# Optimization experiments

Measured on AMD Instinct MI355X. Metric: run time of the kernel, lower is better.

Reference implementation:

```python
import jax, jax.numpy as jnp
import numpy as np

H = 768; NH = 12; HD = 64; LW = 256
NEG = -1e9  # finite stand-in for -inf; exp underflows to 0 identically in fp32 softmax

def setup_inputs() -> dict:
    key = jax.random.key(0)
    ks = jax.random.split(key, 10)
    s = 0.02
    return {
        "x": jax.random.normal(ks[0], (2, 2048, H), dtype=jnp.float32),
        "w_attn": jax.random.normal(ks[1], (H, 3 * H), dtype=jnp.float32) * s,
        "b_attn": jnp.zeros((3 * H,), dtype=jnp.float32),
        "w_proj": jax.random.normal(ks[2], (H, H), dtype=jnp.float32) * s,
        "b_proj": jnp.zeros((H,), dtype=jnp.float32),
        "w_sel1": jax.random.normal(ks[3], (H, H // 4), dtype=jnp.float32) * s,
        "b_sel1": jnp.zeros((H // 4,), dtype=jnp.float32),
        "w_sel2": jax.random.normal(ks[4], (H // 4, 1), dtype=jnp.float32) * s,
        "b_sel2": jnp.zeros((1,), dtype=jnp.float32),
        "local_weight": jnp.float32(0.5),
        "global_weight": jnp.float32(0.5),
    }

def reference(x, w_attn, b_attn, w_proj, b_proj, w_sel1, b_sel1, w_sel2, b_sel2,
              local_weight, global_weight):
    B, T, C = x.shape
    scale = HD ** -0.5
    qkv = x @ w_attn + b_attn                       # [B,T,3C]
    q, k, v = jnp.split(qkv, 3, axis=-1)
    q = q.reshape(B, T, NH, HD).transpose(0, 2, 1, 3)  # [B,H,T,D]
    k = k.reshape(B, T, NH, HD).transpose(0, 2, 1, 3)
    v = v.reshape(B, T, NH, HD).transpose(0, 2, 1, 3)
    scores = jnp.einsum('bhqd,bhkd->bhqk', q, k) * scale  # [B,H,T,T]
    i = jnp.arange(T)[:, None]
    j = jnp.arange(T)[None, :]
    causal = j > i
    scores = jnp.where(causal[None, None], NEG, scores)
    # selectivity: per-key-position gate in [0.2, 1.0]
    sel = jax.nn.sigmoid(jax.nn.gelu(x @ w_sel1 + b_sel1, approximate=False) @ w_sel2 + b_sel2)  # [B,T,1]
    sel = sel[:, None, :, 0][:, :, None, :]            # [B,1,1,T]
    modulated = scores * (0.2 + 0.8 * sel)
    outside_local = j < jnp.clip(i - LW, 0, None)
    local = jnp.where(outside_local[None, None], NEG, scores)
    wl = jax.nn.sigmoid(local_weight)
    wg = jax.nn.sigmoid(global_weight)
    wsum = wl + wg
    wl, wg = wl / wsum, wg / wsum
    attn = wl * jax.nn.softmax(local, axis=-1) + wg * jax.nn.softmax(modulated, axis=-1)
    out = jnp.einsum('bhqk,bhkd->bhqd', attn, v)        # [B,H,T,D]
    out = out.transpose(0, 2, 1, 3).reshape(B, T, C)
    return out @ w_proj + b_proj
```

## Files before the change

### kernel.cpp

```cpp
#include <hip/hip_runtime.h>
#include <cmath>

#define TT    2048
#define CC    768
#define NHEAD 12
#define LWIN  256
#define BBATCH 2
#define MROWS 4096
#define QBA   128
#define KB    64
#define NSLOT 72
#define L2E   1.4426950408889634f

typedef unsigned int u32;
typedef u32 u32x2 __attribute__((ext_vector_type(2)));
typedef u32 u32x4 __attribute__((ext_vector_type(4)));
typedef short bf16x8 __attribute__((ext_vector_type(8)));
typedef float f32x16 __attribute__((ext_vector_type(16)));

union F4 { u32x4 u; bf16x8 h; };

__device__ __forceinline__ unsigned short b16(float a) {
  u32 u = __float_as_uint(a);
  return (unsigned short)((u + 0x7FFFu + ((u >> 16) & 1u)) >> 16);
}
__device__ __forceinline__ u32 pk2(float a, float b) {
  return (u32)b16(a) | ((u32)b16(b) << 16);
}

__global__ __launch_bounds__(256) void cvt_bf16_kernel(
    const float* __restrict__ in, unsigned short* __restrict__ out, int n8) {
  const int i = blockIdx.x * 256 + threadIdx.x;
  if (i >= n8) return;
  const float4 a = *(const float4*)&in[(size_t)i * 8];
  const float4 b = *(const float4*)&in[(size_t)i * 8 + 4];
  u32x4 w = {pk2(a.x, a.y), pk2(a.z, a.w), pk2(b.x, b.y), pk2(b.z, b.w)};
  *(u32x4*)&out[(size_t)i * 8] = w;
}

__global__ __launch_bounds__(256) void transpose_cvt_kernel(
    const float* __restrict__ W, unsigned short* __restrict__ Wt, int K, int N) {
  __shared__ float t[32][33];
  const int tid = threadIdx.x;
  const int n0 = blockIdx.x * 32, k0 = blockIdx.y * 32;
  const int r = tid >> 5, c = tid & 31;
#pragma unroll
  for (int rr = 0; rr < 4; ++rr)
    t[r + 8 * rr][c] = W[(size_t)(k0 + r + 8 * rr) * N + n0 + c];
  __syncthreads();
#pragma unroll
  for (int rr = 0; rr < 4; ++rr)
    Wt[(size_t)(n0 + r + 8 * rr) * K + k0 + c] = b16(t[c][r + 8 * rr]);
}

template <int NT, bool OUTBF, int ACT>
__global__ __launch_bounds__(256) void gemm_mfma_kernel(
    const unsigned short* __restrict__ A, const unsigned short* __restrict__ Bt,
    const float* __restrict__ bias, void* __restrict__ Cout,
    int M, int N, int K) {
  __shared__ alignas(16) unsigned short as_[128 * 64];
  __shared__ alignas(16) unsigned short bs_[NT * 32 * 64];
  const int tid = threadIdx.x;
  const int lane = tid & 63;
  const int wv = tid >> 6;
  const int hi = lane >> 5;
  const int l31 = lane & 31;
  const int m0 = blockIdx.y * 128, n0 = blockIdx.x * (NT * 32);

  u32x4 ar[4], br[NT];

#define G_ISSUE(K0)                                                           \
  do {                                                                        \
    _Pragma("unroll") for (int i = 0; i < 4; ++i) {                           \
      const int idx = tid + (i << 8);                                         \
      const int r = idx >> 3, c = idx & 7;                                    \
      ar[i] = *(const u32x4*)&A[(size_t)(m0 + r) * K + (K0) + c * 8];         \
    }                                                                         \
    _Pragma("unroll") for (int i = 0; i < NT; ++i) {                          \
      const int idx = tid + (i << 8);                                         \
      const int r = idx >> 3, c = idx & 7;                                    \
      br[i] = *(const u32x4*)&Bt[(size_t)(n0 + r) * K + (K0) + c * 8];        \
    }                                                                         \
  } while (0)

#define G_WRITE()                                                             \
  do {                                                                        \
    _Pragma("unroll") for (int i = 0; i < 4; ++i) {                           \
      const int idx = tid + (i << 8);                                         \
      const int r = idx >> 3, c = idx & 7;                                    \
      *(u32x4*)((char*)as_ + r * 128 + ((c ^ (r & 7)) << 4)) = ar[i];         \
    }                                                                         \
    _Pragma("unroll") for (int i = 0; i < NT; ++i) {                          \
      const int idx = tid + (i << 8);                                         \
      const int r = idx >> 3, c = idx & 7;                                    \
      *(u32x4*)((char*)bs_ + r * 128 + ((c ^ (r & 7)) << 4)) = br[i];         \
    }                                                                         \
  } while (0)

  f32x16 acc[NT];
#pragma unroll
  for (int nt = 0; nt < NT; ++nt)
#pragma unroll
    for (int r = 0; r < 16; ++r) acc[nt][r] = 0.f;

  G_ISSUE(0);
  G_WRITE();
  __syncthreads();

  const int arow = wv * 32 + l31;
  for (int k0 = 0; k0 < K; k0 += 64) {
    if (k0 + 64 < K) G_ISSUE(k0 + 64);
#pragma unroll
    for (int s = 0; s < 4; ++s) {
      F4 af;
      af.u = *(const u32x4*)((const char*)as_ + arow * 128 +
                             (((2 * s + hi) ^ (arow & 7)) << 4));
#pragma unroll
      for (int nt = 0; nt < NT; ++nt) {
        F4 bf;
        bf.u = *(const u32x4*)((const char*)bs_ + (nt * 32 + l31) * 128 +
                               (((2 * s + hi) ^ (l31 & 7)) << 4));
        acc[nt] = __builtin_amdgcn_mfma_f32_32x32x16_bf16(af.h, bf.h, acc[nt], 0, 0, 0);
      }
    }
    __syncthreads();
    if (k0 + 64 < K) G_WRITE();
    __syncthreads();
  }

#pragma unroll
  for (int nt = 0; nt < NT; ++nt)
#pragma unroll
    for (int r = 0; r < 16; ++r) {
      const int m = m0 + wv * 32 + (r & 3) + 8 * (r >> 2) + 4 * hi;
      const int n = n0 + nt * 32 + l31;
      float v = acc[nt][r] + bias[n];
      if (ACT == 1) v = 0.5f * v * (1.f + erff(v * 0.70710678118654752f));
      if (OUTBF)
        ((unsigned short*)Cout)[(size_t)m * N + n] = b16(v);
      else
        ((float*)Cout)[(size_t)m * N + n] = v;
    }
#undef G_ISSUE
#undef G_WRITE
}

__global__ __launch_bounds__(256) void gate_kernel(
    const float* __restrict__ gh, const float* __restrict__ w2,
    const float* __restrict__ b2, float* __restrict__ gate) {
  const int lane = threadIdx.x & 63;
  const int row = blockIdx.x * 4 + (threadIdx.x >> 6);
  float s = 0.f;
#pragma unroll
  for (int j = 0; j < 3; ++j) {
    const int c = lane + 64 * j;
    s = fmaf(gh[(size_t)row * 192 + c], w2[c], s);
  }
#pragma unroll
  for (int off = 32; off; off >>= 1) s += __shfl_xor(s, off, 64);
  if (lane == 0) {
    const float sel = 1.f / (1.f + __expf(-(s + b2[0])));
    gate[row] = 0.125f * L2E * (0.2f + 0.8f * sel);
  }
}

__global__ __launch_bounds__(256) void attn_part_kernel(
    const unsigned short* __restrict__ qkvb, const float* __restrict__ gate8,
    unsigned short* __restrict__ part1O, unsigned short* __restrict__ part2O,
    float* __restrict__ part2ML) {
  __shared__ alignas(16) unsigned short k_s[2][KB * 64];
  __shared__ alignas(16) unsigned short vt_s[2][64 * 68];
  __shared__ float g_s[2][KB];

  const int tid = threadIdx.x;
  const int lane = tid & 63;
  const int wv = tid >> 6;
  const int hi = lane >> 5;
  const int l31 = lane & 31;
  const int bh = blockIdx.y;
  const int bb = bh / NHEAD;
  const int hh = bh % NHEAD;

  u32x4 kr[2], vr[2];
  float gr = 0.f;

#define A_ISSUE(T0, WG)                                                        \
  do {                                                                         \
    _Pragma("unroll") for (int i = 0; i < 2; ++i) {                            \
      const int idx = tid + (i << 8);                                          \
      const int r = idx >> 3, c = idx & 7;                                     \
      const size_t base = (size_t)(bb * TT + (T0) + r) * 2304 + hh * 64 + c * 8; \
      kr[i] = *(const u32x4*)&qkvb[base + 768];                                \
      vr[i] = *(const u32x4*)&qkvb[base + 1536];                               \
    }                                                                          \
    if (WG && tid < KB) gr = gate8[bb * TT + (T0) + tid];                      \
  } while (0)

#define A_WRITE(KD, VD, GD, WG)                                                \
  do {                                                                         \
    _Pragma("unroll") for (int i = 0; i < 2; ++i) {                            \
      const int idx = tid + (i << 8);                                          \
      const int r = idx >> 3, c = idx & 7;                                     \
      *(u32x4*)((char*)(KD) + r * 128 + ((c ^ (r & 7)) << 4)) = kr[i];         \
      const int d0 = c * 8;                                                    \
      (VD)[(d0 + 0) * 68 + r] = (unsigned short)(vr[i].x & 0xffff);            \
      (VD)[(d0 + 1) * 68 + r] = (unsigned short)(vr[i].x >> 16);               \
      (VD)[(d0 + 2) * 68 + r] = (unsigned short)(vr[i].y & 0xffff);            \
      (VD)[(d0 + 3) * 68 + r] = (unsigned short)(vr[i].y >> 16);               \
      (VD)[(d0 + 4) * 68 + r] = (unsigned short)(vr[i].z & 0xffff);            \
      (VD)[(d0 + 5) * 68 + r] = (unsigned short)(vr[i].z >> 16);               \
      (VD)[(d0 + 6) * 68 + r] = (unsigned short)(vr[i].w & 0xffff);            \
      (VD)[(d0 + 7) * 68 + r] = (unsigned short)(vr[i].w >> 16);               \
    }                                                                          \
    if (WG && tid < KB) (GD)[tid] = gr;                                        \
  } while (0)

#define QK_MFMA(KC)                                                            \
  do {                                                                         \
    _Pragma("unroll") for (int s = 0; s < 4; ++s) {                            \
      const int blk = (2 * s + hi) ^ (l31 & 7);                                \
      F4 f0, f1;                                                               \
      f0.u = *(const u32x4*)((const char*)(KC) + l31 * 128 + (blk << 4));      \
      f1.u = *(const u32x4*)((const char*)(KC) + (32 + l31) * 128 + (blk << 4));\
      S0 = __builtin_amdgcn_mfma_f32_32x32x16_bf16(f0.h, qf[s], S0, 0, 0, 0);  \
      S1 = __builtin_amdgcn_mfma_f32_32x32x16_bf16(f1.h, qf[s], S1, 0, 0, 0);  \
    }                                                                          \
  } while (0)

#define V_FRAGS(VC)                                                            \
  do {                                                                         \
    const char* vb0 = (const char*)(VC) + (size_t)l31 * 136 + hi * 8;          \
    const char* vb1 = vb0 + 32 * 136;                                          \
    _Pragma("unroll") for (int kb4 = 0; kb4 < 4; ++kb4) {                      \
      const u32x2 a0 = *(const u32x2*)(vb0 + 32 * kb4);                        \
      const u32x2 a1 = *(const u32x2*)(vb0 + 32 * kb4 + 16);                   \
      va[kb4].u = (u32x4){a0.x, a0.y, a1.x, a1.y};                             \
      const u32x2 c0 = *(const u32x2*)(vb1 + 32 * kb4);                        \
      const u32x2 c1 = *(const u32x2*)(vb1 + 32 * kb4 + 16);                   \
      vbf[kb4].u = (u32x4){c0.x, c0.y, c1.x, c1.y};                            \
    }                                                                          \
  } while (0)

#define SOFTMAX_PV(M, L, OA, OB)                                               \
  do {                                                                         \
    float red[8];                                                              \
    _Pragma("unroll") for (int i = 0; i < 8; ++i)                              \
      red[i] = fmaxf(fmaxf(S0[i], S0[i + 8]), fmaxf(S1[i], S1[i + 8]));        \
    _Pragma("unroll") for (int off = 4; off; off >>= 1)                        \
      _Pragma("unroll") for (int i = 0; i < off; ++i)                          \
        red[i] = fmaxf(red[i], red[i + off]);                                  \
    const float pmax = fmaxf(red[0], __shfl_xor(red[0], 32));                  \
    const int resc = __any(pmax > M + 8.f);                                    \
    float f = 1.f;                                                             \
    if (resc) {                                                                \
      const float mn = fmaxf(M, pmax);                                         \
      f = exp2f(M - mn);                                                       \
      M = mn;                                                                  \
    }                                                                          \
    _Pragma("unroll") for (int r = 0; r < 16; ++r) {                           \
      S0[r] = exp2f(S0[r] - M);                                                \
      S1[r] = exp2f(S1[r] - M);                                                \
    }                                                                          \
    _Pragma("unroll") for (int i = 0; i < 8; ++i)                              \
      red[i] = (S0[i] + S0[i + 8]) + (S1[i] + S1[i + 8]);                      \
    _Pragma("unroll") for (int off = 4; off; off >>= 1)                        \
      _Pragma("unroll") for (int i = 0; i < off; ++i)                          \
        red[i] += red[i + off];                                                \
    const float sum = red[0] + __shfl_xor(red[0], 32);                         \
    if (resc) {                                                                \
      L = L * f + sum;                                                         \
      _Pragma("unroll") for (int r = 0; r < 16; ++r) {                         \
        const float fq = __shfl(f, (r & 3) + 8 * (r >> 2) + 4 * hi);           \
        OA[r] *= fq;                                                           \
        OB[r] *= fq;                                                           \
      }                                                                        \
    } else {                                                                   \
      L += sum;                                                                \
    }                                                                          \
    u32 Pp[16];                                                                \
    _Pragma("unroll") for (int w = 0; w < 8; ++w) {                            \
      asm("v_cvt_pk_bf16_f32 %0, %1, %2" : "=v"(Pp[w]) : "v"(S0[2 * w]), "v"(S0[2 * w + 1])); \
      asm("v_cvt_pk_bf16_f32 %0, %1, %2" : "=v"(Pp[8 + w]) : "v"(S1[2 * w]), "v"(S1[2 * w + 1])); \
    }                                                                          \
    _Pragma("unroll") for (int kb4 = 0; kb4 < 4; ++kb4) {                      \
      F4 a;                                                                    \
      a.u = (u32x4){Pp[4 * kb4 + 0], Pp[4 * kb4 + 1], Pp[4 * kb4 + 2],         \
                    Pp[4 * kb4 + 3]};                                          \
      OA = __builtin_amdgcn_mfma_f32_32x32x16_bf16(a.h, va[kb4].h, OA, 0, 0, 0);\
      OB = __builtin_amdgcn_mfma_f32_32x32x16_bf16(a.h, vbf[kb4].h, OB, 0, 0, 0);\
    }                                                                          \
  } while (0)

  if (blockIdx.x < NSLOT) {
    const int slot = (NSLOT - 1) - blockIdx.x;
    const int g = (slot < 2) ? 0 : (slot < 6) ? 1 : (slot < 12) ? 2 :
                  (slot < 20) ? 3 : (slot < 30) ? 4 : (slot < 42) ? 5 :
                  (slot < 56) ? 6 : 7;
    const int idxg = slot - g * (g + 1);
    const int e = (idxg >= g + 1) ? 1 : 0;
    const int qt = 2 * g + e;
    const int ch = idxg - e * (g + 1);
    const int r0 = qt * QBA;
    const int r0w = r0 + wv * 32;
    const int iq = r0w + l31;
    const int tlo = ch * 4;
    const int thi = min(tlo + 4, 2 * (qt + 1));

    bf16x8 qf[4];
    {
      const size_t qrow = (size_t)(bb * TT + r0w + l31) * 2304 + hh * 64;
#pragma unroll
      for (int s = 0; s < 4; ++s) {
        F4 f;
        f.u = *(const u32x4*)&qkvb[qrow + 16 * s + 8 * hi];
        qf[s] = f.h;
      }
    }

    float m2 = -1e30f, l2 = 0.f;
    f32x16 O2a, O2b;
#pragma unroll
    for (int r = 0; r < 16; ++r) { O2a[r] = 0.f; O2b[r] = 0.f; }

    A_ISSUE(tlo * 64, 1);
    A_WRITE(k_s[0], vt_s[0], g_s[0], 1);
    __syncthreads();

    int cur = 0;
    for (int t = tlo; t < thi; ++t) {
      const int t0 = t << 6;
      if (t + 1 < thi) A_ISSUE((t + 1) * 64, 1);
      if (t0 <= r0w + 31) {
        f32x16 S0, S1;
#pragma unroll
        for (int r = 0; r < 16; ++r) { S0[r] = 0.f; S1[r] = 0.f; }
        QK_MFMA(k_s[cur]);
        F4 va[4], vbf[4];
        V_FRAGS(vt_s[cur]);
#pragma unroll
        for (int r = 0; r < 16; ++r) {
          const int crow = (r & 3) + 8 * (r >> 2) + 4 * hi;
          const int k0 = t0 + crow;
          S0[r] = (k0 <= iq) ? S0[r] * g_s[cur][crow] : -1e30f;
          S1[r] = (k0 + 32 <= iq) ? S1[r] * g_s[cur][32 + crow] : -1e30f;
        }
        SOFTMAX_PV(m2, l2, O2a, O2b);
      }
      if (t + 1 < thi) A_WRITE(k_s[cur ^ 1], vt_s[cur ^ 1], g_s[cur ^ 1], 1);
      __syncthreads();
      cur ^= 1;
    }

    const size_t srow = ((size_t)bh * NSLOT + slot) * 128 + wv * 32;
    if (hi == 0) {
      float2 ml;
      ml.x = m2;
      ml.y = l2;
      *(float2*)&part2ML[(srow + l31) * 2] = ml;
    }
#pragma unroll
    for (int r = 0; r < 16; ++r) {
      const int crow = (r & 3) + 8 * (r >> 2) + 4 * hi;
      const size_t rowi = srow + crow;
      part2O[rowi * 64 + l31]      = b16(O2a[r]);
      part2O[rowi * 64 + 32 + l31] = b16(O2b[r]);
    }
  } else {
    const int qt = blockIdx.x - NSLOT;
    const int r0 = qt * QBA;
    const int r0w = r0 + wv * 32;
    const int iq = r0w + l31;
    int tlo = (r0 - LWIN) >> 6;
    tlo = tlo < 0 ? 0 : tlo;
    const int thi = (r0 + QBA) >> 6;

    bf16x8 qf[4];
    {
      const size_t qrow = (size_t)(bb * TT + r0w + l31) * 2304 + hh * 64;
#pragma unroll
      for (int s = 0; s < 4; ++s) {
        F4 f;
        f.u = *(const u32x4*)&qkvb[qrow + 16 * s + 8 * hi];
        qf[s] = f.h;
      }
    }

    float m1 = -1e30f, l1 = 0.f;
    f32x16 O1a, O1b;
#pragma unroll
    for (int r = 0; r < 16; ++r) { O1a[r] = 0.f; O1b[r] = 0.f; }

    A_ISSUE(tlo * 64, 0);
    A_WRITE(k_s[0], vt_s[0], g_s[0], 0);
    __syncthreads();

    int cur = 0;
    for (int t = tlo; t < thi; ++t) {
      const int t0 = t << 6;
      if (t + 1 < thi) A_ISSUE((t + 1) * 64, 0);
      if (t0 + 63 >= r0w - LWIN && t0 <= r0w + 31) {
        f32x16 S0, S1;
#pragma unroll
        for (int r = 0; r < 16; ++r) { S0[r] = 0.f; S1[r] = 0.f; }
        QK_MFMA(k_s[cur]);
        F4 va[4], vbf[4];
        V_FRAGS(vt_s[cur]);
#pragma unroll
        for (int r = 0; r < 16; ++r) {
          const int crow = (r & 3) + 8 * (r >> 2) + 4 * hi;
          const int k0 = t0 + crow;
          const bool ok0 = (k0 <= iq) && (k0 + LWIN >= iq);
          const bool ok1 = (k0 + 32 <= iq) && (k0 + 32 + LWIN >= iq);
          S0[r] = ok0 ? S0[r] * (0.125f * L2E) : -1e30f;
          S1[r] = ok1 ? S1[r] * (0.125f * L2E) : -1e30f;
        }
        SOFTMAX_PV(m1, l1, O1a, O1b);
      }
      if (t + 1 < thi) A_WRITE(k_s[cur ^ 1], vt_s[cur ^ 1], g_s[cur ^ 1], 0);
      __syncthreads();
      cur ^= 1;
    }

    const size_t obase = (((size_t)bh * 16 + qt) * 128 + wv * 32) * 64;
#pragma unroll
    for (int r = 0; r < 16; ++r) {
      const int crow = (r & 3) + 8 * (r >> 2) + 4 * hi;
      const float inv = 1.f / __shfl(l1, crow);
      part1O[obase + (size_t)crow * 64 + l31]      = b16(O1a[r] * inv);
      part1O[obase + (size_t)crow * 64 + 32 + l31] = b16(O1b[r] * inv);
    }
  }
#undef A_ISSUE
#undef A_WRITE
#undef QK_MFMA
#undef V_FRAGS
#undef SOFTMAX_PV
}

__global__ __launch_bounds__(256) void combine_kernel(
    const unsigned short* __restrict__ part1O,
    const unsigned short* __restrict__ part2O,
    const float* __restrict__ part2ML,
    const float* __restrict__ lwp, const float* __restrict__ gwp,
    unsigned short* __restrict__ aob) {
  const int t = blockIdx.x * 256 + threadIdx.x;
  const int d2 = t & 31;
  const int rr = t >> 5;
  const int bh = rr >> 11;
  const int qrow = rr & 2047;
  const int qt = qrow >> 7, row = qrow & 127;
  const int g = qt >> 1;
  const int sb = g * (g + 1) + (qt & 1) * (g + 1);
  const int nc = g + 1;

  const u32 o1p = *(const u32*)&part1O[((((size_t)bh * 16 + qt) * 128 + row) << 6) + 2 * d2];

  float m = -1e30f, l = 0.f, oa = 0.f, ob = 0.f;
  for (int c = 0; c < nc; ++c) {
    const size_t rowi = ((size_t)bh * NSLOT + sb + c) * 128 + row;
    const float2 ml = *(const float2*)&part2ML[rowi * 2];
    const u32 po = *(const u32*)&part2O[(rowi << 6) + 2 * d2];
    const float mn = fmaxf(m, ml.x);
    const float e0 = exp2f(m - mn), e1 = exp2f(ml.x - mn);
    l = l * e0 + ml.y * e1;
    oa = oa * e0 + __uint_as_float(po << 16) * e1;
    ob = ob * e0 + __uint_as_float(po & 0xffff0000u) * e1;
    m = mn;
  }
  const float wlr = 1.f / (1.f + __expf(-lwp[0]));
  const float wgr = 1.f / (1.f + __expf(-gwp[0]));
  const float wl = wlr / (wlr + wgr);
  const float wg = wgr / (wlr + wgr);
  const float s2 = wg / l;
  const float outa = wl * __uint_as_float(o1p << 16) + oa * s2;
  const float outb = wl * __uint_as_float(o1p & 0xffff0000u) + ob * s2;
  const int bb = bh / NHEAD, hh = bh % NHEAD;
  *(u32*)&aob[(size_t)(bb * TT + qrow) * CC + hh * 64 + 2 * d2] = pk2(outa, outb);
}

extern "C" void kernel_launch(void* const* d_in, const int* in_sizes, int n_in,
                              void* d_out, int out_size, void* d_ws, size_t ws_size,
                              hipStream_t stream) {
  const float* x      = (const float*)d_in[0];
  const float* w_attn = (const float*)d_in[1];
  const float* b_attn = (const float*)d_in[2];
  const float* w_proj = (const float*)d_in[3];
  const float* b_proj = (const float*)d_in[4];
  const float* w_sel1 = (const float*)d_in[5];
  const float* b_sel1 = (const float*)d_in[6];
  const float* w_sel2 = (const float*)d_in[7];
  const float* b_sel2 = (const float*)d_in[8];
  const float* lw     = (const float*)d_in[9];
  const float* gw     = (const float*)d_in[10];
  float* out = (float*)d_out;

  unsigned short* qkvb  = (unsigned short*)d_ws;
  unsigned short* xb    = qkvb + (size_t)MROWS * 2304;
  unsigned short* wta   = xb + (size_t)MROWS * 768;
  unsigned short* wtp   = wta + (size_t)2304 * 768;
  unsigned short* wts   = wtp + (size_t)768 * 768;
  unsigned short* aob   = wts + (size_t)192 * 768;
  unsigned short* part1O = aob + (size_t)MROWS * 768;
  unsigned short* part2O = part1O + (size_t)24 * 16 * 128 * 64;
  float* gatebuf = (float*)(part2O + (size_t)24 * NSLOT * 128 * 64);
  float* part2ML = gatebuf + MROWS;
  float* ghbuf   = part2ML + (size_t)24 * NSLOT * 128 * 2;

  cvt_bf16_kernel<<<(MROWS * 768 / 8 + 255) / 256, 256, 0, stream>>>(
      x, xb, MROWS * 768 / 8);
  transpose_cvt_kernel<<<dim3(2304 / 32, 768 / 32), 256, 0, stream>>>(
      w_attn, wta, 768, 2304);
  transpose_cvt_kernel<<<dim3(768 / 32, 768 / 32), 256, 0, stream>>>(
      w_proj, wtp, 768, 768);
  transpose_cvt_kernel<<<dim3(192 / 32, 768 / 32), 256, 0, stream>>>(
      w_sel1, wts, 768, 192);
  gemm_mfma_kernel<2, false, 1><<<dim3(192 / 64, MROWS / 128), 256, 0, stream>>>(
      xb, wts, b_sel1, ghbuf, MROWS, 192, 768);
  gate_kernel<<<MROWS / 4, 256, 0, stream>>>(ghbuf, w_sel2, b_sel2, gatebuf);
  gemm_mfma_kernel<4, true, 0><<<dim3(2304 / 128, MROWS / 128), 256, 0, stream>>>(
      xb, wta, b_attn, qkvb, MROWS, 2304, 768);
  attn_part_kernel<<<dim3(NSLOT + 16, BBATCH * NHEAD), 256, 0, stream>>>(
      qkvb, gatebuf, part1O, part2O, part2ML);
  combine_kernel<<<(BBATCH * NHEAD * TT * 32) / 256, 256, 0, stream>>>(
      part1O, part2O, part2ML, lw, gw, aob);
  gemm_mfma_kernel<2, false, 0><<<dim3(768 / 64, MROWS / 128), 256, 0, stream>>>(
      aob, wtp, b_proj, out, MROWS, 768, 768);
}
```

Measured before the change: 162.7 us.

## Skip masking on interior tiles, reorder attention blocks, vectorize combine kernel

The attention kernel now takes a mask-free path for key tiles that lie entirely inside the causal or local window, so it skips the per-element comparisons and selects. Block indices are remapped so the 16 local-window blocks get the lowest block IDs and the global slots follow, which changes scheduling order. The combine kernel now handles 8 bf16 values per thread with 128-bit loads and stores, cutting its thread count by a factor of four and reducing per-element address and partial-ML load overhead. This adds branch divergence risk between tiles and increases register use in combine.

```diff
diff --git a/kernel.cpp b/kernel.cpp
--- a/kernel.cpp
+++ b/kernel.cpp
@@ -291,8 +291,8 @@
     }                                                                          \
   } while (0)
 
-  if (blockIdx.x < NSLOT) {
-    const int slot = (NSLOT - 1) - blockIdx.x;
+  if (blockIdx.x >= 16) {
+    const int slot = (NSLOT - 1) - (blockIdx.x - 16);
     const int g = (slot < 2) ? 0 : (slot < 6) ? 1 : (slot < 12) ? 2 :
                   (slot < 20) ? 3 : (slot < 30) ? 4 : (slot < 42) ? 5 :
                   (slot < 56) ? 6 : 7;
@@ -337,12 +337,21 @@
         QK_MFMA(k_s[cur]);
         F4 va[4], vbf[4];
         V_FRAGS(vt_s[cur]);
-#pragma unroll
-        for (int r = 0; r < 16; ++r) {
-          const int crow = (r & 3) + 8 * (r >> 2) + 4 * hi;
-          const int k0 = t0 + crow;
-          S0[r] = (k0 <= iq) ? S0[r] * g_s[cur][crow] : -1e30f;
-          S1[r] = (k0 + 32 <= iq) ? S1[r] * g_s[cur][32 + crow] : -1e30f;
+        if (t0 + 63 <= r0w) {
+#pragma unroll
+          for (int r = 0; r < 16; ++r) {
+            const int crow = (r & 3) + 8 * (r >> 2) + 4 * hi;
+            S0[r] *= g_s[cur][crow];
+            S1[r] *= g_s[cur][32 + crow];
+          }
+        } else {
+#pragma unroll
+          for (int r = 0; r < 16; ++r) {
+            const int crow = (r & 3) + 8 * (r >> 2) + 4 * hi;
+            const int k0 = t0 + crow;
+            S0[r] = (k0 <= iq) ? S0[r] * g_s[cur][crow] : -1e30f;
+            S1[r] = (k0 + 32 <= iq) ? S1[r] * g_s[cur][32 + crow] : -1e30f;
+          }
         }
         SOFTMAX_PV(m2, l2, O2a, O2b);
       }
@@ -366,7 +375,7 @@
       part2O[rowi * 64 + 32 + l31] = b16(O2b[r]);
     }
   } else {
-    const int qt = blockIdx.x - NSLOT;
+    const int qt = blockIdx.x;
     const int r0 = qt * QBA;
     const int r0w = r0 + wv * 32;
     const int iq = r0w + l31;
@@ -405,14 +414,22 @@
         QK_MFMA(k_s[cur]);
         F4 va[4], vbf[4];
         V_FRAGS(vt_s[cur]);
-#pragma unroll
-        for (int r = 0; r < 16; ++r) {
-          const int crow = (r & 3) + 8 * (r >> 2) + 4 * hi;
-          const int k0 = t0 + crow;
-          const bool ok0 = (k0 <= iq) && (k0 + LWIN >= iq);
-          const bool ok1 = (k0 + 32 <= iq) && (k0 + 32 + LWIN >= iq);
-          S0[r] = ok0 ? S0[r] * (0.125f * L2E) : -1e30f;
-          S1[r] = ok1 ? S1[r] * (0.125f * L2E) : -1e30f;
+        if (t0 + 63 <= r0w && t0 >= r0w + 31 - LWIN) {
+#pragma unroll
+          for (int r = 0; r < 16; ++r) {
+            S0[r] *= (0.125f * L2E);
+            S1[r] *= (0.125f * L2E);
+          }
+        } else {
+#pragma unroll
+          for (int r = 0; r < 16; ++r) {
+            const int crow = (r & 3) + 8 * (r >> 2) + 4 * hi;
+            const int k0 = t0 + crow;
+            const bool ok0 = (k0 <= iq) && (k0 + LWIN >= iq);
+            const bool ok1 = (k0 + 32 <= iq) && (k0 + 32 + LWIN >= iq);
+            S0[r] = ok0 ? S0[r] * (0.125f * L2E) : -1e30f;
+            S1[r] = ok1 ? S1[r] * (0.125f * L2E) : -1e30f;
+          }
         }
         SOFTMAX_PV(m1, l1, O1a, O1b);
       }
@@ -444,8 +461,8 @@
     const float* __restrict__ lwp, const float* __restrict__ gwp,
     unsigned short* __restrict__ aob) {
   const int t = blockIdx.x * 256 + threadIdx.x;
-  const int d2 = t & 31;
-  const int rr = t >> 5;
+  const int d8 = t & 7;
+  const int rr = t >> 3;
   const int bh = rr >> 11;
   const int qrow = rr & 2047;
   const int qt = qrow >> 7, row = qrow & 127;
@@ -453,29 +470,40 @@
   const int sb = g * (g + 1) + (qt & 1) * (g + 1);
   const int nc = g + 1;
 
-  const u32 o1p = *(const u32*)&part1O[((((size_t)bh * 16 + qt) * 128 + row) << 6) + 2 * d2];
-
-  float m = -1e30f, l = 0.f, oa = 0.f, ob = 0.f;
+  float m = -1e30f, l = 0.f;
+  float oa[4], ob[4];
+#pragma unroll
+  for (int j = 0; j < 4; ++j) { oa[j] = 0.f; ob[j] = 0.f; }
+
   for (int c = 0; c < nc; ++c) {
     const size_t rowi = ((size_t)bh * NSLOT + sb + c) * 128 + row;
     const float2 ml = *(const float2*)&part2ML[rowi * 2];
-    const u32 po = *(const u32*)&part2O[(rowi << 6) + 2 * d2];
+    const u32x4 po = *(const u32x4*)&part2O[(rowi << 6) + 8 * d8];
     const float mn = fmaxf(m, ml.x);
     const float e0 = exp2f(m - mn), e1 = exp2f(ml.x - mn);
     l = l * e0 + ml.y * e1;
-    oa = oa * e0 + __uint_as_float(po << 16) * e1;
-    ob = ob * e0 + __uint_as_float(po & 0xffff0000u) * e1;
+#pragma unroll
+    for (int j = 0; j < 4; ++j) {
+      oa[j] = oa[j] * e0 + __uint_as_float(po[j] << 16) * e1;
+      ob[j] = ob[j] * e0 + __uint_as_float(po[j] & 0xffff0000u) * e1;
+    }
     m = mn;
   }
+  const u32x4 o1p = *(const u32x4*)&part1O[((((size_t)bh * 16 + qt) * 128 + row) << 6) + 8 * d8];
   const float wlr = 1.f / (1.f + __expf(-lwp[0]));
   const float wgr = 1.f / (1.f + __expf(-gwp[0]));
   const float wl = wlr / (wlr + wgr);
   const float wg = wgr / (wlr + wgr);
   const float s2 = wg / l;
-  const float outa = wl * __uint_as_float(o1p << 16) + oa * s2;
-  const float outb = wl * __uint_as_float(o1p & 0xffff0000u) + ob * s2;
+  u32x4 outw;
+#pragma unroll
+  for (int j = 0; j < 4; ++j) {
+    const float outa = wl * __uint_as_float(o1p[j] << 16) + oa[j] * s2;
+    const float outb = wl * __uint_as_float(o1p[j] & 0xffff0000u) + ob[j] * s2;
+    outw[j] = pk2(outa, outb);
+  }
   const int bb = bh / NHEAD, hh = bh % NHEAD;
-  *(u32*)&aob[(size_t)(bb * TT + qrow) * CC + hh * 64 + 2 * d2] = pk2(outa, outb);
+  *(u32x4*)&aob[(size_t)(bb * TT + qrow) * CC + hh * 64 + 8 * d8] = outw;
 }
 
 extern "C" void kernel_launch(void* const* d_in, const int* in_sizes, int n_in,
@@ -521,7 +549,7 @@
       xb, wta, b_attn, qkvb, MROWS, 2304, 768);
   attn_part_kernel<<<dim3(NSLOT + 16, BBATCH * NHEAD), 256, 0, stream>>>(
       qkvb, gatebuf, part1O, part2O, part2ML);
-  combine_kernel<<<(BBATCH * NHEAD * TT * 32) / 256, 256, 0, stream>>>(
+  combine_kernel<<<(BBATCH * NHEAD * TT * 8) / 256, 256, 0, stream>>>(
       part1O, part2O, part2ML, lw, gw, aob);
   gemm_mfma_kernel<2, false, 0><<<dim3(768 / 64, MROWS / 128), 256, 0, stream>>>(
       aob, wtp, b_proj, out, MROWS, 768, 768);
```

New measurement: 141.9 us. 1.15x faster.
